# Performance work log

Hardware: AMD Instinct MI355X
Metric: run time of the kernel (lower is better)

## Reference

```python
import jax, jax.numpy as jnp
import numpy as np

B, NB, C, FEAT = 2, 512, 80, 1024
FIRST_N = 128
NMS_FC = 128
POS_EMB = 64
GROUPS = 16
ATT_D = (1024, 1024, 128)
NUM_THRESH = 3
BBOX_W = (10.0, 10.0, 5.0, 5.0)
SCALE_CLAMP = float(np.log(1000.0 / 16.0))


def setup_inputs() -> dict:
    key = jax.random.key(0)
    ks = jax.random.split(key, 24)
    roi_feat = jax.random.normal(ks[0], (B * NB, FEAT), jnp.float32)
    scores = jax.random.normal(ks[1], (B * NB, C + 1), jnp.float32)
    proposal_deltas = jax.random.normal(ks[2], (B * NB, C * 4), jnp.float32) * 0.5
    xy = jax.random.uniform(ks[3], (B * NB, 2), jnp.float32) * 800.0
    wh = jax.random.uniform(ks[4], (B * NB, 2), jnp.float32) * 100.0 + 1.0
    proposal_boxes = jnp.concatenate([xy, xy + wh], axis=1)

    def lin(k, fin, fout, std=0.01):
        return jax.random.normal(k, (fin, fout), jnp.float32) * std

    return {
        'roi_feat': roi_feat,
        'scores': scores,
        'proposal_deltas': proposal_deltas,
        'proposal_boxes': proposal_boxes,
        'roi_w': lin(ks[5], FEAT, NMS_FC), 'roi_b': jnp.zeros((NMS_FC,), jnp.float32),
        'rank_w': lin(ks[6], FEAT, NMS_FC), 'rank_b': jnp.zeros((NMS_FC,), jnp.float32),
        'logit_w': lin(ks[7], NMS_FC, NUM_THRESH), 'logit_b': jnp.full((NUM_THRESH,), -3.0, jnp.float32),
        'pos_w': lin(ks[8], POS_EMB, GROUPS), 'pos_b': jnp.zeros((GROUPS,), jnp.float32),
        'q_w': lin(ks[9], NMS_FC, ATT_D[0]), 'q_b': jnp.zeros((ATT_D[0],), jnp.float32),
        'k_w': lin(ks[10], NMS_FC, ATT_D[1]), 'k_b': jnp.zeros((ATT_D[1],), jnp.float32),
        'out_w': jax.random.normal(ks[11], (GROUPS, NMS_FC, ATT_D[2] // GROUPS), jnp.float32) * 0.01,
        'out_b': jnp.zeros((ATT_D[2],), jnp.float32),
        'num_boxes': NB,
    }


def _rank_embedding():
    # sinusoidal rank embedding, dim FEAT
    fr = jnp.arange(FEAT // 2, dtype=jnp.float32)
    dim_mat = jnp.power(1000.0, (2.0 / FEAT) * fr)
    div = jnp.arange(FIRST_N, dtype=jnp.float32)[:, None] / dim_mat[None, :]
    return jnp.concatenate([jnp.sin(div), jnp.cos(div)], axis=1)  # (FIRST_N, FEAT)


def _pos_embed(boxes):
    # boxes: (FIRST_N, C, 4) -> (C, N, N, POS_EMB)
    b = jnp.transpose(boxes, (1, 0, 2))  # (C, N, 4)
    x1, y1, x2, y2 = b[..., 0], b[..., 1], b[..., 2], b[..., 3]
    w = x2 - x1 + 1.0
    h = y2 - y1 + 1.0
    cx = 0.5 * (x1 + x2)
    cy = 0.5 * (y1 + y2)
    dx = jnp.log(jnp.maximum(jnp.abs((cx[:, :, None] - cx[:, None, :]) / w[:, :, None]), 1e-3))
    dy = jnp.log(jnp.maximum(jnp.abs((cy[:, :, None] - cy[:, None, :]) / h[:, :, None]), 1e-3))
    dw = jnp.log(w[:, :, None] / w[:, None, :])
    dh = jnp.log(h[:, :, None] / h[:, None, :])
    pm = jnp.stack([dx, dy, dw, dh], axis=-1)  # (C, N, N, 4)
    fr = jnp.arange(POS_EMB // 8, dtype=jnp.float32)
    dim_mat = jnp.power(1000.0, (8.0 / POS_EMB) * fr)
    dv = (pm * 100.0)[..., None] / dim_mat  # (C, N, N, 4, POS_EMB//8)
    e = jnp.concatenate([jnp.sin(dv), jnp.cos(dv)], axis=-1)  # (C, N, N, 4, POS_EMB//4)
    return e.reshape(pm.shape[:3] + (POS_EMB,))


def reference(roi_feat, scores, proposal_deltas, proposal_boxes,
              roi_w, roi_b, rank_w, rank_b, logit_w, logit_b,
              pos_w, pos_b, q_w, q_b, k_w, k_b, out_w, out_b, num_boxes):
    deltas = jax.lax.stop_gradient(proposal_deltas)  # detached in original
    pboxes = jax.lax.stop_gradient(proposal_boxes)
    batch = deltas.shape[0] // num_boxes

    # ---- Box2BoxTransform.apply_deltas ----
    widths = pboxes[:, 2] - pboxes[:, 0]
    heights = pboxes[:, 3] - pboxes[:, 1]
    ctr_x = pboxes[:, 0] + 0.5 * widths
    ctr_y = pboxes[:, 1] + 0.5 * heights
    wx, wy, ww, wh = BBOX_W
    d = deltas.reshape(-1, C, 4)
    dx = d[..., 0] / wx
    dy = d[..., 1] / wy
    dw = jnp.minimum(d[..., 2] / ww, SCALE_CLAMP)
    dh = jnp.minimum(d[..., 3] / wh, SCALE_CLAMP)
    pcx = dx * widths[:, None] + ctr_x[:, None]
    pcy = dy * heights[:, None] + ctr_y[:, None]
    pw = jnp.exp(dw) * widths[:, None]
    ph = jnp.exp(dh) * heights[:, None]
    refined = jnp.stack([pcx - 0.5 * pw, pcy - 0.5 * ph, pcx + 0.5 * pw, pcy + 0.5 * ph], axis=-1)
    refined = refined.reshape(batch, num_boxes, C, 4)

    # ---- softmax + per-class descending sort, keep first_n ----
    sc = scores.reshape(batch, num_boxes, C + 1)
    probs = jax.nn.softmax(sc[..., :C], axis=1)
    rank_idxs = jnp.argsort(-probs, axis=1)[:, :FIRST_N, :]  # (B, FIRST_N, C)
    sorted_score = jnp.take_along_axis(probs, rank_idxs, axis=1)  # (B, FIRST_N, C)
    sorted_boxes = jax.vmap(lambda bx, i: jnp.take_along_axis(bx, i[..., None], axis=0))(refined, rank_idxs)  # (B, FIRST_N, C, 4)

    # ---- rank + roi embeddings ----
    rank_feat = _rank_embedding() @ rank_w + rank_b  # (FIRST_N, NMS_FC)
    roi_emb = (roi_feat @ roi_w + roi_b).reshape(batch, num_boxes, NMS_FC)
    sorted_roi = jax.vmap(lambda e, i: e[i])(roi_emb, rank_idxs)  # (B, FIRST_N, C, NMS_FC)
    emb_feat = sorted_roi + rank_feat[None, :, None, :]

    dq = ATT_D[0] // GROUPS
    dk = ATT_D[1] // GROUPS

    def attend(feat, boxes):
        # feat: (FIRST_N, C, NMS_FC), boxes: (FIRST_N, C, 4)
        pe = _pos_embed(boxes)  # (C, N, N, POS_EMB)
        aff_w = jax.nn.relu(pe @ pos_w + pos_b)  # (C, N, N, G)
        aff_w = jnp.transpose(aff_w, (0, 3, 1, 2))  # (C, G, N, N)
        f = jnp.transpose(feat, (1, 0, 2))  # (C, N, NMS_FC)
        q = (f @ q_w + q_b).reshape(C, FIRST_N, GROUPS, dq).transpose(0, 2, 1, 3)
        k = (f @ k_w + k_b).reshape(C, FIRST_N, GROUPS, dk).transpose(0, 2, 1, 3)
        aff = jnp.einsum('cgnd,cgmd->cgnm', q, k) / jnp.sqrt(jnp.float32(dk))
        sm = jax.nn.softmax(jnp.log(jnp.maximum(aff_w, 1e-6)) + aff, axis=-1)
        ov = jnp.einsum('cgnm,cmd->cgnd', sm, f)  # (C, G, N, NMS_FC)
        lin = jnp.einsum('cgnd,gde->cnge', ov, out_w).reshape(C, FIRST_N, ATT_D[2]) + out_b
        return jnp.transpose(lin, (1, 0, 2))  # (N, C, ATT_D[2])

    att = jax.vmap(attend)(emb_feat, sorted_boxes)
    all_feat = jax.nn.relu(emb_feat + att)
    logit = all_feat @ logit_w + logit_b  # (B, FIRST_N, C, NUM_THRESH)
    nms_multi_score = jax.nn.sigmoid(logit) * sorted_score[..., None]
    return nms_multi_score
```

## Files before the change

kernel.cpp:

```cpp
#include <hip/hip_runtime.h>
#include <math.h>

#define B_    2
#define NB_   512
#define C_    80
#define FEAT_ 1024
#define FN_   128
#define FC_   128
#define PE_   64
#define G_    16
#define DQ_   64
#define EO_   8
#define NT_   3
#define SCALE_CLAMP_ 4.135166556742356f

typedef __attribute__((ext_vector_type(8))) short bf16x8;
typedef __attribute__((ext_vector_type(4))) float f32x4;

#define O_ROIP    ((size_t)0)
#define O_RANKP   (O_ROIP + (size_t)2*B_*NB_*FC_)
#define O_RANKIDX (O_RANKP + (size_t)2*FN_*FC_)
#define O_SSCORE  (O_RANKIDX + (size_t)B_*FN_*C_)
#define O_SBOX    (O_SSCORE + (size_t)B_*FN_*C_)
#define O_EMB     (O_SBOX + (size_t)B_*FN_*C_*4)
#define O_ATT     (O_EMB + (size_t)B_*FN_*C_*FC_)
#define O_LW      (O_ATT + (size_t)B_*FN_*C_*FC_)

__device__ __forceinline__ float bf2f(unsigned short u) {
    return __uint_as_float(((unsigned int)u) << 16);
}
__device__ __forceinline__ unsigned short f2bf(float f) {
    unsigned int x = __float_as_uint(f);
    unsigned int r = (x + 0x7fff + ((x >> 16) & 1)) >> 16;
    return (unsigned short)r;
}

#define ADDR128(row, gr)  ((row)*128 + ((((gr) ^ ((row)&7))) << 4))
#define ADDR256(row, gr)  ((row)*256 + ((((gr) ^ ((row)&15))) << 4))

__global__ __launch_bounds__(256) void k_embed(const float* __restrict__ roi_feat,
                                               const float* __restrict__ roi_w,
                                               const float* __restrict__ roi_b,
                                               const float* __restrict__ rank_w,
                                               const float* __restrict__ rank_b,
                                               float* __restrict__ roiP,
                                               float* __restrict__ rankP)
{
    const int bid = blockIdx.x;
    const int kh  = bid & 1;
    const int rt  = bid >> 1;
    const bool isRank = rt >= 64;
    const int row0 = (isRank ? rt - 64 : rt) * 16;
    const int t = threadIdx.x;
    const int w = t >> 6, lane = t & 63, lr = lane & 15, lh = lane >> 4;
    const int col0 = w * 32;
    const float* W = isRank ? rank_w : roi_w;
    const float* bias = isRank ? rank_b : roi_b;

    const int arow = row0 + lr;
    f32x4 acc0 = {0,0,0,0}, acc1 = {0,0,0,0};

    #pragma unroll 4
    for (int ks = 0; ks < 16; ++ks) {
        const int kb = kh*512 + ks*32 + lh*8;
        bf16x8 af;
        if (!isRank) {
            float4 a0 = *(const float4*)(roi_feat + (size_t)arow*FEAT_ + kb);
            float4 a1 = *(const float4*)(roi_feat + (size_t)arow*FEAT_ + kb + 4);
            af[0] = (short)f2bf(a0.x); af[1] = (short)f2bf(a0.y);
            af[2] = (short)f2bf(a0.z); af[3] = (short)f2bf(a0.w);
            af[4] = (short)f2bf(a1.x); af[5] = (short)f2bf(a1.y);
            af[6] = (short)f2bf(a1.z); af[7] = (short)f2bf(a1.w);
        } else {
            #pragma unroll
            for (int j = 0; j < 8; ++j) {
                int k = kb + j;
                int kk = k & 511;
                float inv = exp2f(-(float)kk * 0.0194644226f);
                float arg = (float)arow * inv;
                float v = (k < 512) ? __sinf(arg) : __cosf(arg);
                af[j] = (short)f2bf(v);
            }
        }
        bf16x8 bf0, bf1;
        #pragma unroll
        for (int j = 0; j < 8; ++j) {
            const float* wr = W + (size_t)(kb + j)*FC_ + col0 + lr;
            bf0[j] = (short)f2bf(wr[0]);
            bf1[j] = (short)f2bf(wr[16]);
        }
        acc0 = __builtin_amdgcn_mfma_f32_16x16x32_bf16(af, bf0, acc0, 0, 0, 0);
        acc1 = __builtin_amdgcn_mfma_f32_16x16x32_bf16(af, bf1, acc1, 0, 0, 0);
    }
    float* dst = isRank ? (rankP + (size_t)kh*FN_*FC_) : (roiP + (size_t)kh*(B_*NB_)*FC_);
    #pragma unroll
    for (int tile = 0; tile < 2; ++tile) {
        f32x4 a = tile ? acc1 : acc0;
        int col = col0 + tile*16 + lr;
        float bv = (kh == 0) ? bias[col] : 0.0f;
        #pragma unroll
        for (int reg = 0; reg < 4; ++reg) {
            int rr = row0 + lh*4 + reg;
            dst[(size_t)rr*FC_ + col] = a[reg] + bv;
        }
    }
}

__global__ __launch_bounds__(512) void k_topk(const float* __restrict__ scores,
                                              int* __restrict__ rank_idx,
                                              float* __restrict__ sorted_score)
{
    int b = blockIdx.x / C_, c = blockIdx.x % C_;
    __shared__ float p[NB_];
    __shared__ float red[NB_];
    int i = threadIdx.x;
    float s = scores[(size_t)(b*NB_ + i)*(C_+1) + c];
    red[i] = s; __syncthreads();
    for (int o = 256; o > 0; o >>= 1) { if (i < o) red[i] = fmaxf(red[i], red[i+o]); __syncthreads(); }
    float mx = red[0]; __syncthreads();
    float e = expf(s - mx);
    red[i] = e; __syncthreads();
    for (int o = 256; o > 0; o >>= 1) { if (i < o) red[i] += red[i+o]; __syncthreads(); }
    float sum = red[0]; __syncthreads();
    float pi = e / sum;
    p[i] = pi; __syncthreads();
    int rank = 0;
    for (int j = 0; j < NB_; ++j) {
        float pj = p[j];
        rank += (pj > pi) || (pj == pi && j < i);
    }
    if (rank < FN_) {
        rank_idx[(size_t)(b*FN_ + rank)*C_ + c] = i;
        sorted_score[(size_t)(b*FN_ + rank)*C_ + c] = pi;
    }
}

__global__ __launch_bounds__(256) void k_gather(const int* __restrict__ rank_idx,
                                                const float* __restrict__ roiP,
                                                const float* __restrict__ rankP,
                                                const float* __restrict__ pdeltas,
                                                const float* __restrict__ pboxes,
                                                float* __restrict__ emb_feat,
                                                float* __restrict__ sorted_boxes)
{
    const int t = threadIdx.x;
    const int item = blockIdx.x*8 + (t >> 5);
    const int l = t & 31;
    const int c = item % C_;
    const int bn = item / C_;
    const int n = bn & (FN_-1);
    const int b = bn >> 7;
    const int idx = rank_idx[item];
    const int row = b*NB_ + idx;
    float4 e0 = *(const float4*)(roiP + (size_t)row*FC_ + l*4);
    float4 e1 = *(const float4*)(roiP + (size_t)(B_*NB_ + row)*FC_ + l*4);
    float4 r0 = *(const float4*)(rankP + (size_t)n*FC_ + l*4);
    float4 r1 = *(const float4*)(rankP + (size_t)(FN_ + n)*FC_ + l*4);
    *(float4*)(emb_feat + (size_t)item*FC_ + l*4) =
        make_float4(e0.x+e1.x+r0.x+r1.x, e0.y+e1.y+r0.y+r1.y,
                    e0.z+e1.z+r0.z+r1.z, e0.w+e1.w+r0.w+r1.w);
    if (l == 0) {
        float x1 = pboxes[row*4+0], y1 = pboxes[row*4+1], x2 = pboxes[row*4+2], y2 = pboxes[row*4+3];
        float w = x2 - x1, h = y2 - y1;
        float cx = x1 + 0.5f*w, cy = y1 + 0.5f*h;
        const float* dl = pdeltas + (size_t)row*(C_*4) + c*4;
        float dx = dl[0]/10.0f, dy = dl[1]/10.0f;
        float dw = fminf(dl[2]/5.0f, SCALE_CLAMP_);
        float dh = fminf(dl[3]/5.0f, SCALE_CLAMP_);
        float pcx = dx*w + cx, pcy = dy*h + cy;
        float pw = expf(dw)*w, ph = expf(dh)*h;
        float* ob = sorted_boxes + (size_t)item*4;
        ob[0] = pcx - 0.5f*pw; ob[1] = pcy - 0.5f*ph;
        ob[2] = pcx + 0.5f*pw; ob[3] = pcy + 0.5f*ph;
    }
}

__global__ __launch_bounds__(256) void k_pos2(const float* __restrict__ sorted_boxes,
                                              const float* __restrict__ pos_w,
                                              const float* __restrict__ pos_b,
                                              unsigned short* __restrict__ lw)
{
    const int n2   = blockIdx.x & 63;
    const int rest = blockIdx.x >> 6;
    const int cl   = rest % C_;
    const int b    = rest / C_;
    const int n0   = n2 * 2;
    const int t    = threadIdx.x;

    __shared__ float geomL[FN_][6];
    __shared__ unsigned short featL[256*PE_];
    __shared__ unsigned short poswL[G_*PE_];
    __shared__ float pbL[G_];
    __shared__ float sdimL[8];

    if (t < FN_) {
        const float* bx = sorted_boxes + (((size_t)(b*FN_ + t))*C_ + cl)*4;
        float x1 = bx[0], y1 = bx[1], x2 = bx[2], y2 = bx[3];
        float w = x2 - x1 + 1.0f;
        float h = y2 - y1 + 1.0f;
        geomL[t][0] = 0.5f*(x1+x2);
        geomL[t][1] = 0.5f*(y1+y2);
        geomL[t][2] = w;
        geomL[t][3] = h;
        geomL[t][4] = __logf(w);
        geomL[t][5] = __logf(h);
    } else {
        int id = t - 128;
        int g  = id >> 3;
        int gr = id & 7;
        unsigned short u[8];
        #pragma unroll
        for (int j = 0; j < 8; ++j) u[j] = f2bf(pos_w[(gr*8 + j)*G_ + g]);
        *(uint4*)((char*)poswL + ADDR128(g, gr)) =
            make_uint4((unsigned)u[0] | ((unsigned)u[1] << 16),
                       (unsigned)u[2] | ((unsigned)u[3] << 16),
                       (unsigned)u[4] | ((unsigned)u[5] << 16),
                       (unsigned)u[6] | ((unsigned)u[7] << 16));
    }
    if (t < G_) pbL[t] = pos_b[t];
    if (t >= 16 && t < 24) sdimL[t-16] = 1.0f / powf(1000.0f, 0.125f*(float)(t-16));
    __syncthreads();

    {
        const int nl = t >> 7;
        const int m  = t & 127;
        const int n  = n0 + nl;
        float pm[4];
        {
            float cxn = geomL[n][0], cyn = geomL[n][1];
            float rwn = 1.0f/geomL[n][2], rhn = 1.0f/geomL[n][3];
            pm[0] = __logf(fmaxf(fabsf((cxn - geomL[m][0]) * rwn), 1e-3f)) * 100.0f;
            pm[1] = __logf(fmaxf(fabsf((cyn - geomL[m][1]) * rhn), 1e-3f)) * 100.0f;
            pm[2] = (geomL[n][4] - geomL[m][4]) * 100.0f;
            pm[3] = (geomL[n][5] - geomL[m][5]) * 100.0f;
        }
        char* base = (char*)featL;
        #pragma unroll
        for (int f = 0; f < 4; ++f) {
            float s[8], c[8];
            #pragma unroll
            for (int r = 0; r < 8; ++r) {
                __sincosf(pm[f] * sdimL[r], &s[r], &c[r]);
            }
            unsigned short us[8], uc[8];
            #pragma unroll
            for (int r = 0; r < 8; ++r) { us[r] = f2bf(s[r]); uc[r] = f2bf(c[r]); }
            *(uint4*)(base + ADDR128(t, 2*f)) =
                make_uint4((unsigned)us[0] | ((unsigned)us[1] << 16),
                           (unsigned)us[2] | ((unsigned)us[3] << 16),
                           (unsigned)us[4] | ((unsigned)us[5] << 16),
                           (unsigned)us[6] | ((unsigned)us[7] << 16));
            *(uint4*)(base + ADDR128(t, 2*f + 1)) =
                make_uint4((unsigned)uc[0] | ((unsigned)uc[1] << 16),
                           (unsigned)uc[2] | ((unsigned)uc[3] << 16),
                           (unsigned)uc[4] | ((unsigned)uc[5] << 16),
                           (unsigned)uc[6] | ((unsigned)uc[7] << 16));
        }
    }
    __syncthreads();

    {
        const int wave = t >> 6, lane = t & 63;
        const int lr = lane & 15, lh = lane >> 4;
        const float pbg = pbL[lr];
        #pragma unroll
        for (int ti = 0; ti < 4; ++ti) {
            const int t16 = wave*4 + ti;
            f32x4 acc = {0,0,0,0};
            #pragma unroll
            for (int ks = 0; ks < 2; ++ks) {
                bf16x8 a  = *(const bf16x8*)((char*)featL + ADDR128(t16*16 + lr, ks*4 + lh));
                bf16x8 bb = *(const bf16x8*)((char*)poswL + ADDR128(lr, ks*4 + lh));
                acc = __builtin_amdgcn_mfma_f32_16x16x32_bf16(a, bb, acc, 0, 0, 0);
            }
            const int g = lr;
            #pragma unroll
            for (int reg = 0; reg < 4; ++reg) {
                int p = t16*16 + lh*4 + reg;
                int n = n0 + (p >> 7);
                int m = p & 127;
                float w = fmaxf(fmaxf(acc[reg] + pbg, 0.0f), 1e-6f);
                lw[(((size_t)(b*C_ + cl)*FN_ + n)*G_ + g)*FN_ + m] = f2bf(w);
            }
        }
    }
}

#define FT_OFF   0
#define QL_OFF   32768
#define KL_OFF   49152
#define WT_OFF   65536
#define AFF_OFF  65536
#define VT_OFF   133632
#define BIAS_OFF 137728
#define SMEM_SZ  138240

__global__ __launch_bounds__(1024) void k_attn(const float* __restrict__ emb_feat,
                                               const float* __restrict__ q_w, const float* __restrict__ q_b,
                                               const float* __restrict__ k_w, const float* __restrict__ k_b,
                                               const float* __restrict__ out_w, const float* __restrict__ out_b,
                                               const unsigned short* __restrict__ lw,
                                               float* __restrict__ att)
{
    const int g    = blockIdx.x & 15;
    const int rest = blockIdx.x >> 4;
    const int cl   = rest % C_;
    const int b    = rest / C_;
    const int c    = cl;
    const int t  = threadIdx.x;
    const int wave = t >> 6;
    const int lane = t & 63;
    const int lr = lane & 15;
    const int lh = lane >> 4;

    __shared__ char smem[SMEM_SZ];
    float* biasL = (float*)(smem + BIAS_OFF);
    float* affF  = (float*)(smem + AFF_OFF);

    for (int s = 0; s < 4; ++s) {
        int fi = t + s*1024;
        int n  = fi >> 5;
        int d4 = (fi & 31) << 2;
        float4 v = *(const float4*)(emb_feat + ((size_t)(b*FN_ + n)*C_ + c)*FC_ + d4);
        char* dst = smem + FT_OFF + ADDR256(n, d4 >> 3) + ((d4 >> 2) & 1)*8;
        *(uint2*)dst = make_uint2((unsigned)f2bf(v.x) | ((unsigned)f2bf(v.y) << 16),
                                  (unsigned)f2bf(v.z) | ((unsigned)f2bf(v.w) << 16));
    }
    for (int s = 0; s < 2; ++s) {
        int id = t + s*1024;
        int r  = id & 127;
        int g8 = id >> 7;
        const float* src = (r < 64) ? (q_w + (size_t)(g8*8)*1024 + g*DQ_ + r)
                                    : (k_w + (size_t)(g8*8)*1024 + g*DQ_ + (r-64));
        unsigned short u[8];
        #pragma unroll
        for (int j = 0; j < 8; ++j) u[j] = f2bf(src[(size_t)j*1024]);
        char* dst = smem + WT_OFF + ADDR256(r, g8);
        *(uint4*)dst = make_uint4((unsigned)u[0] | ((unsigned)u[1] << 16),
                                  (unsigned)u[2] | ((unsigned)u[3] << 16),
                                  (unsigned)u[4] | ((unsigned)u[5] << 16),
                                  (unsigned)u[6] | ((unsigned)u[7] << 16));
    }
    if (t < 128) {
        int e  = t & 7;
        int g8 = t >> 3;
        const float* src = out_w + (size_t)g*FC_*EO_ + (size_t)(g8*8)*EO_ + e;
        unsigned short u[8];
        #pragma unroll
        for (int j = 0; j < 8; ++j) u[j] = f2bf(src[(size_t)j*EO_]);
        int r = 128 + e;
        char* dst = smem + WT_OFF + ADDR256(r, g8);
        *(uint4*)dst = make_uint4((unsigned)u[0] | ((unsigned)u[1] << 16),
                                  (unsigned)u[2] | ((unsigned)u[3] << 16),
                                  (unsigned)u[4] | ((unsigned)u[5] << 16),
                                  (unsigned)u[6] | ((unsigned)u[7] << 16));
    }
    if (t >= 256 && t < 512) {
        int i = t - 256;
        *(uint2*)(smem + WT_OFF + 136*256 + i*8) = make_uint2(0u, 0u);
    }
    if (t >= 512 && t < 768) {
        int i = t - 512;
        *(uint2*)(smem + VT_OFF + 8*256 + i*8) = make_uint2(0u, 0u);
    }
    if (t >= 128 && t < 256) {
        int r = t - 128;
        biasL[r] = (r < 64) ? q_b[g*DQ_ + r] : k_b[g*DQ_ + (r-64)];
    }
    __syncthreads();

    {
        const int rb = (wave >> 2) * 32;
        const int nb = (wave & 3) * 32;
        f32x4 acc00 = {0,0,0,0}, acc01 = {0,0,0,0}, acc10 = {0,0,0,0}, acc11 = {0,0,0,0};
        f32x4 accV  = {0,0,0,0};
        #pragma unroll
        for (int ks = 0; ks < 4; ++ks) {
            int soff = ((ks*4 + lh) ^ lr) << 4;
            bf16x8 a0 = *(const bf16x8*)(smem + WT_OFF + (rb + lr)*256 + soff);
            bf16x8 a1 = *(const bf16x8*)(smem + WT_OFF + (rb + 16 + lr)*256 + soff);
            bf16x8 b0 = *(const bf16x8*)(smem + FT_OFF + (nb + lr)*256 + soff);
            bf16x8 b1 = *(const bf16x8*)(smem + FT_OFF + (nb + 16 + lr)*256 + soff);
            acc00 = __builtin_amdgcn_mfma_f32_16x16x32_bf16(a0, b0, acc00, 0, 0, 0);
            acc01 = __builtin_amdgcn_mfma_f32_16x16x32_bf16(a0, b1, acc01, 0, 0, 0);
            acc10 = __builtin_amdgcn_mfma_f32_16x16x32_bf16(a1, b0, acc10, 0, 0, 0);
            acc11 = __builtin_amdgcn_mfma_f32_16x16x32_bf16(a1, b1, acc11, 0, 0, 0);
            if (wave < 8) {
                bf16x8 av = *(const bf16x8*)(smem + WT_OFF + (128 + lr)*256 + soff);
                bf16x8 bv = *(const bf16x8*)(smem + FT_OFF + (wave*16 + lr)*256 + soff);
                accV = __builtin_amdgcn_mfma_f32_16x16x32_bf16(av, bv, accV, 0, 0, 0);
            }
        }
        #pragma unroll
        for (int ti = 0; ti < 2; ++ti) {
            #pragma unroll
            for (int tj = 0; tj < 2; ++tj) {
                f32x4 a = (ti == 0) ? (tj == 0 ? acc00 : acc01) : (tj == 0 ? acc10 : acc11);
                int r0 = rb + ti*16 + lh*4;
                int n  = nb + tj*16 + lr;
                float v0 = a[0] + biasL[r0+0];
                float v1 = a[1] + biasL[r0+1];
                float v2 = a[2] + biasL[r0+2];
                float v3 = a[3] + biasL[r0+3];
                int dq0 = r0 & 63;
                int off = (r0 < 64 ? QL_OFF : KL_OFF);
                char* dst = smem + off + ADDR128(n, dq0 >> 3) + ((dq0 >> 2) & 1)*8;
                *(uint2*)dst = make_uint2((unsigned)f2bf(v0) | ((unsigned)f2bf(v1) << 16),
                                          (unsigned)f2bf(v2) | ((unsigned)f2bf(v3) << 16));
            }
        }
        if (wave < 8 && lh < 2) {
            int m = wave*16 + lr;
            #pragma unroll
            for (int reg = 0; reg < 4; ++reg) {
                int e = lh*4 + reg;
                char* dst = smem + VT_OFF + (e)*256 + ((((m >> 3) ^ e)) << 4) + (m & 7)*2;
                *(unsigned short*)dst = f2bf(accV[reg]);
            }
        }
    }
    __syncthreads();

    {
        const int nb = (wave >> 2) * 32;
        const int mb = (wave & 3) * 32;
        f32x4 acc00 = {0,0,0,0}, acc01 = {0,0,0,0}, acc10 = {0,0,0,0}, acc11 = {0,0,0,0};
        #pragma unroll
        for (int ks = 0; ks < 2; ++ks) {
            int soff = ((ks*4 + lh) ^ (lr & 7)) << 4;
            bf16x8 a0 = *(const bf16x8*)(smem + QL_OFF + (nb + lr)*128 + soff);
            bf16x8 a1 = *(const bf16x8*)(smem + QL_OFF + (nb + 16 + lr)*128 + soff);
            bf16x8 b0 = *(const bf16x8*)(smem + KL_OFF + (mb + lr)*128 + soff);
            bf16x8 b1 = *(const bf16x8*)(smem + KL_OFF + (mb + 16 + lr)*128 + soff);
            acc00 = __builtin_amdgcn_mfma_f32_16x16x32_bf16(a0, b0, acc00, 0, 0, 0);
            acc01 = __builtin_amdgcn_mfma_f32_16x16x32_bf16(a0, b1, acc01, 0, 0, 0);
            acc10 = __builtin_amdgcn_mfma_f32_16x16x32_bf16(a1, b0, acc10, 0, 0, 0);
            acc11 = __builtin_amdgcn_mfma_f32_16x16x32_bf16(a1, b1, acc11, 0, 0, 0);
        }
        #pragma unroll
        for (int ti = 0; ti < 2; ++ti) {
            #pragma unroll
            for (int tj = 0; tj < 2; ++tj) {
                f32x4 a = (ti == 0) ? (tj == 0 ? acc00 : acc01) : (tj == 0 ? acc10 : acc11);
                int n0 = nb + ti*16 + lh*4;
                int m  = mb + tj*16 + lr;
                #pragma unroll
                for (int reg = 0; reg < 4; ++reg)
                    affF[(n0 + reg)*133 + m] = a[reg];
            }
        }
    }
    __syncthreads();

    {
        const int row = t >> 3;
        const int lp  = t & 7;
        const int m0  = lp * 16;
        const unsigned short* lwrow = lw + ((((size_t)(b*C_ + cl))*FN_ + row)*G_ + g)*FN_ + m0;
        float v[16];
        float mx = -INFINITY;
        #pragma unroll
        for (int j = 0; j < 16; ++j) {
            float val = affF[row*133 + m0 + j]*0.125f + __logf(bf2f(lwrow[j]));
            v[j] = val;
            mx = fmaxf(mx, val);
        }
        #pragma unroll
        for (int s = 1; s < 8; s <<= 1) mx = fmaxf(mx, __shfl_xor(mx, s, 8));
        float sum = 0.f;
        #pragma unroll
        for (int j = 0; j < 16; ++j) { v[j] = __expf(v[j] - mx); sum += v[j]; }
        #pragma unroll
        for (int s = 1; s < 8; s <<= 1) sum += __shfl_xor(sum, s, 8);
        float rs = 1.0f / sum;
        unsigned short u[16];
        #pragma unroll
        for (int j = 0; j < 16; ++j) u[j] = f2bf(v[j] * rs);
        char* d0 = smem + FT_OFF + ADDR256(row, lp*2);
        char* d1 = smem + FT_OFF + ADDR256(row, lp*2 + 1);
        *(uint4*)d0 = make_uint4((unsigned)u[0] | ((unsigned)u[1] << 16),
                                 (unsigned)u[2] | ((unsigned)u[3] << 16),
                                 (unsigned)u[4] | ((unsigned)u[5] << 16),
                                 (unsigned)u[6] | ((unsigned)u[7] << 16));
        *(uint4*)d1 = make_uint4((unsigned)u[8]  | ((unsigned)u[9]  << 16),
                                 (unsigned)u[10] | ((unsigned)u[11] << 16),
                                 (unsigned)u[12] | ((unsigned)u[13] << 16),
                                 (unsigned)u[14] | ((unsigned)u[15] << 16));
    }
    __syncthreads();

    if (wave < 8) {
        const int tb = wave * 16;
        f32x4 acc = {0,0,0,0};
        #pragma unroll
        for (int ks = 0; ks < 4; ++ks) {
            int soff = ((ks*4 + lh) ^ lr) << 4;
            bf16x8 a = *(const bf16x8*)(smem + FT_OFF + (tb + lr)*256 + soff);
            bf16x8 bv = *(const bf16x8*)(smem + VT_OFF + lr*256 + soff);
            acc = __builtin_amdgcn_mfma_f32_16x16x32_bf16(a, bv, acc, 0, 0, 0);
        }
        if (lr < 8) {
            float ob = out_b[g*EO_ + lr];
            #pragma unroll
            for (int reg = 0; reg < 4; ++reg) {
                int n = tb + lh*4 + reg;
                att[((size_t)(b*FN_ + n)*C_ + c)*FC_ + g*EO_ + lr] = acc[reg] + ob;
            }
        }
    }
}

__global__ __launch_bounds__(256) void k_final(const float* __restrict__ emb_feat,
                                               const float* __restrict__ att,
                                               const float* __restrict__ logit_w,
                                               const float* __restrict__ logit_b,
                                               const float* __restrict__ sorted_score,
                                               float* __restrict__ out)
{
    __shared__ float lwL[FC_*NT_ + NT_];
    const int t = threadIdx.x;
    for (int i = t; i < FC_*NT_ + NT_; i += 256)
        lwL[i] = (i < FC_*NT_) ? logit_w[i] : logit_b[i - FC_*NT_];
    __syncthreads();
    const int item = blockIdx.x*8 + (t >> 5);
    const int l = t & 31;
    const int d0 = l*4;
    float4 ev = *(const float4*)(emb_feat + (size_t)item*FC_ + d0);
    float4 av = *(const float4*)(att + (size_t)item*FC_ + d0);
    float a0 = fmaxf(ev.x + av.x, 0.f);
    float a1 = fmaxf(ev.y + av.y, 0.f);
    float a2 = fmaxf(ev.z + av.z, 0.f);
    float a3 = fmaxf(ev.w + av.w, 0.f);
    float s0 = a0*lwL[(d0+0)*NT_+0] + a1*lwL[(d0+1)*NT_+0] + a2*lwL[(d0+2)*NT_+0] + a3*lwL[(d0+3)*NT_+0];
    float s1 = a0*lwL[(d0+0)*NT_+1] + a1*lwL[(d0+1)*NT_+1] + a2*lwL[(d0+2)*NT_+1] + a3*lwL[(d0+3)*NT_+1];
    float s2 = a0*lwL[(d0+0)*NT_+2] + a1*lwL[(d0+1)*NT_+2] + a2*lwL[(d0+2)*NT_+2] + a3*lwL[(d0+3)*NT_+2];
    #pragma unroll
    for (int s = 1; s < 32; s <<= 1) {
        s0 += __shfl_xor(s0, s, 32);
        s1 += __shfl_xor(s1, s, 32);
        s2 += __shfl_xor(s2, s, 32);
    }
    if (l < NT_) {
        float lg = (l == 0) ? s0 : (l == 1) ? s1 : s2;
        lg += lwL[FC_*NT_ + l];
        float sg = 1.f / (1.f + expf(-lg));
        out[(size_t)item*NT_ + l] = sg * sorted_score[item];
    }
}

extern "C" void kernel_launch(void* const* d_in, const int* in_sizes, int n_in,
                              void* d_out, int out_size, void* d_ws, size_t ws_size,
                              hipStream_t stream) {
    (void)in_sizes; (void)n_in; (void)out_size; (void)ws_size;
    const float* roi_feat = (const float*)d_in[0];
    const float* scores   = (const float*)d_in[1];
    const float* pdeltas  = (const float*)d_in[2];
    const float* pboxes   = (const float*)d_in[3];
    const float* roi_w    = (const float*)d_in[4];
    const float* roi_b    = (const float*)d_in[5];
    const float* rank_w   = (const float*)d_in[6];
    const float* rank_b   = (const float*)d_in[7];
    const float* logit_w  = (const float*)d_in[8];
    const float* logit_b  = (const float*)d_in[9];
    const float* pos_w    = (const float*)d_in[10];
    const float* pos_b    = (const float*)d_in[11];
    const float* q_w      = (const float*)d_in[12];
    const float* q_b      = (const float*)d_in[13];
    const float* k_w      = (const float*)d_in[14];
    const float* k_b      = (const float*)d_in[15];
    const float* out_w    = (const float*)d_in[16];
    const float* out_b    = (const float*)d_in[17];
    float* ws = (float*)d_ws;

    float* roiP         = ws + O_ROIP;
    float* rankP        = ws + O_RANKP;
    int*   rank_idx     = (int*)(ws + O_RANKIDX);
    float* sorted_score = ws + O_SSCORE;
    float* sorted_boxes = ws + O_SBOX;
    float* emb_feat     = ws + O_EMB;
    float* att          = ws + O_ATT;
    unsigned short* lwb = (unsigned short*)(ws + O_LW);

    k_embed<<<dim3(144), dim3(256), 0, stream>>>(roi_feat, roi_w, roi_b, rank_w, rank_b,
                                                 roiP, rankP);
    k_topk<<<dim3(B_*C_), dim3(512), 0, stream>>>(scores, rank_idx, sorted_score);
    k_gather<<<dim3(B_*FN_*C_/8), dim3(256), 0, stream>>>(rank_idx, roiP, rankP,
                                                          pdeltas, pboxes, emb_feat, sorted_boxes);
    k_pos2<<<dim3(B_*C_*64), dim3(256), 0, stream>>>(sorted_boxes, pos_w, pos_b, lwb);
    k_attn<<<dim3(B_*C_*G_), dim3(1024), 0, stream>>>(emb_feat, q_w, q_b, k_w, k_b,
                                                      out_w, out_b, lwb, att);
    k_final<<<dim3(B_*FN_*C_/8), dim3(256), 0, stream>>>(emb_feat, att, logit_w, logit_b,
                                                         sorted_score, d_out ? (float*)d_out : nullptr);
}
```

Baseline: 180.3 us.

## Shrink attention LDS footprint and precompute log position weights in fp16

The attention kernel no longer stages Q/K/out weights in shared memory. Each wave now loads those weights straight from global memory into MFMA operands. The feature tile moves to a padded 272-byte row layout, and the fp32 affinity scratch becomes fp16 stored in the same buffer, cutting LDS from about 138KB to about 72KB so more blocks can be resident. The position-weight kernel now stores log(w) as fp16 instead of bf16 w, which takes the log out of the softmax inner loop and vectorises the loads. The rank loop also reads the shared scores as float4. The costs are repeated uncoalesced global weight loads per wave and fp16 range and precision risk on the affinities.

```diff
diff --git a/kernel.cpp b/kernel.cpp
--- a/kernel.cpp
+++ b/kernel.cpp
@@ -34,9 +34,16 @@
     unsigned int r = (x + 0x7fff + ((x >> 16) & 1)) >> 16;
     return (unsigned short)r;
 }
+__device__ __forceinline__ unsigned short f2h(float x) {
+    _Float16 h = (_Float16)x;
+    return __builtin_bit_cast(unsigned short, h);
+}
+__device__ __forceinline__ float h2f(unsigned short u) {
+    _Float16 h = __builtin_bit_cast(_Float16, u);
+    return (float)h;
+}
 
 #define ADDR128(row, gr)  ((row)*128 + ((((gr) ^ ((row)&7))) << 4))
-#define ADDR256(row, gr)  ((row)*256 + ((((gr) ^ ((row)&15))) << 4))
 
 __global__ __launch_bounds__(256) void k_embed(const float* __restrict__ roi_feat,
                                                const float* __restrict__ roi_w,
@@ -125,9 +132,13 @@
     float pi = e / sum;
     p[i] = pi; __syncthreads();
     int rank = 0;
-    for (int j = 0; j < NB_; ++j) {
-        float pj = p[j];
-        rank += (pj > pi) || (pj == pi && j < i);
+    for (int j4 = 0; j4 < NB_/4; ++j4) {
+        float4 pj = *(const float4*)&p[j4*4];
+        int j = j4*4;
+        rank += (pj.x > pi) || (pj.x == pi && (j+0) < i);
+        rank += (pj.y > pi) || (pj.y == pi && (j+1) < i);
+        rank += (pj.z > pi) || (pj.z == pi && (j+2) < i);
+        rank += (pj.w > pi) || (pj.w == pi && (j+3) < i);
     }
     if (rank < FN_) {
         rank_idx[(size_t)(b*FN_ + rank)*C_ + c] = i;
@@ -280,22 +291,20 @@
                 int n = n0 + (p >> 7);
                 int m = p & 127;
                 float w = fmaxf(fmaxf(acc[reg] + pbg, 0.0f), 1e-6f);
-                lw[(((size_t)(b*C_ + cl)*FN_ + n)*G_ + g)*FN_ + m] = f2bf(w);
+                lw[(((size_t)(b*C_ + cl)*FN_ + n)*G_ + g)*FN_ + m] = f2h(__logf(w));
             }
         }
     }
 }
 
 #define FT_OFF   0
-#define QL_OFF   32768
-#define KL_OFF   49152
-#define WT_OFF   65536
-#define AFF_OFF  65536
-#define VT_OFF   133632
-#define BIAS_OFF 137728
-#define SMEM_SZ  138240
-
-__global__ __launch_bounds__(1024) void k_attn(const float* __restrict__ emb_feat,
+#define QL_OFF   34816
+#define KL_OFF   51200
+#define VT_OFF   67584
+#define BIAS_OFF 71680
+#define SMEM_SZ  72192
+
+__global__ __launch_bounds__(1024, 8) void k_attn(const float* __restrict__ emb_feat,
                                                const float* __restrict__ q_w, const float* __restrict__ q_b,
                                                const float* __restrict__ k_w, const float* __restrict__ k_b,
                                                const float* __restrict__ out_w, const float* __restrict__ out_b,
@@ -315,49 +324,15 @@
 
     __shared__ char smem[SMEM_SZ];
     float* biasL = (float*)(smem + BIAS_OFF);
-    float* affF  = (float*)(smem + AFF_OFF);
 
     for (int s = 0; s < 4; ++s) {
         int fi = t + s*1024;
         int n  = fi >> 5;
         int d4 = (fi & 31) << 2;
         float4 v = *(const float4*)(emb_feat + ((size_t)(b*FN_ + n)*C_ + c)*FC_ + d4);
-        char* dst = smem + FT_OFF + ADDR256(n, d4 >> 3) + ((d4 >> 2) & 1)*8;
+        char* dst = smem + FT_OFF + n*272 + (fi & 31)*8;
         *(uint2*)dst = make_uint2((unsigned)f2bf(v.x) | ((unsigned)f2bf(v.y) << 16),
                                   (unsigned)f2bf(v.z) | ((unsigned)f2bf(v.w) << 16));
-    }
-    for (int s = 0; s < 2; ++s) {
-        int id = t + s*1024;
-        int r  = id & 127;
-        int g8 = id >> 7;
-        const float* src = (r < 64) ? (q_w + (size_t)(g8*8)*1024 + g*DQ_ + r)
-                                    : (k_w + (size_t)(g8*8)*1024 + g*DQ_ + (r-64));
-        unsigned short u[8];
-        #pragma unroll
-        for (int j = 0; j < 8; ++j) u[j] = f2bf(src[(size_t)j*1024]);
-        char* dst = smem + WT_OFF + ADDR256(r, g8);
-        *(uint4*)dst = make_uint4((unsigned)u[0] | ((unsigned)u[1] << 16),
-                                  (unsigned)u[2] | ((unsigned)u[3] << 16),
-                                  (unsigned)u[4] | ((unsigned)u[5] << 16),
-                                  (unsigned)u[6] | ((unsigned)u[7] << 16));
-    }
-    if (t < 128) {
-        int e  = t & 7;
-        int g8 = t >> 3;
-        const float* src = out_w + (size_t)g*FC_*EO_ + (size_t)(g8*8)*EO_ + e;
-        unsigned short u[8];
-        #pragma unroll
-        for (int j = 0; j < 8; ++j) u[j] = f2bf(src[(size_t)j*EO_]);
-        int r = 128 + e;
-        char* dst = smem + WT_OFF + ADDR256(r, g8);
-        *(uint4*)dst = make_uint4((unsigned)u[0] | ((unsigned)u[1] << 16),
-                                  (unsigned)u[2] | ((unsigned)u[3] << 16),
-                                  (unsigned)u[4] | ((unsigned)u[5] << 16),
-                                  (unsigned)u[6] | ((unsigned)u[7] << 16));
-    }
-    if (t >= 256 && t < 512) {
-        int i = t - 256;
-        *(uint2*)(smem + WT_OFF + 136*256 + i*8) = make_uint2(0u, 0u);
     }
     if (t >= 512 && t < 768) {
         int i = t - 512;
@@ -372,22 +347,33 @@
     {
         const int rb = (wave >> 2) * 32;
         const int nb = (wave & 3) * 32;
+        const float* wsrc = (rb < 64) ? q_w : k_w;
+        const int col0 = g*DQ_ + (rb & 63) + lr;
         f32x4 acc00 = {0,0,0,0}, acc01 = {0,0,0,0}, acc10 = {0,0,0,0}, acc11 = {0,0,0,0};
         f32x4 accV  = {0,0,0,0};
         #pragma unroll
         for (int ks = 0; ks < 4; ++ks) {
-            int soff = ((ks*4 + lh) ^ lr) << 4;
-            bf16x8 a0 = *(const bf16x8*)(smem + WT_OFF + (rb + lr)*256 + soff);
-            bf16x8 a1 = *(const bf16x8*)(smem + WT_OFF + (rb + 16 + lr)*256 + soff);
-            bf16x8 b0 = *(const bf16x8*)(smem + FT_OFF + (nb + lr)*256 + soff);
-            bf16x8 b1 = *(const bf16x8*)(smem + FT_OFF + (nb + 16 + lr)*256 + soff);
+            const int k0 = ks*32 + lh*8;
+            bf16x8 a0, a1;
+            #pragma unroll
+            for (int j = 0; j < 8; ++j) {
+                const float* kp = wsrc + (size_t)(k0 + j)*1024;
+                a0[j] = (short)f2bf(kp[col0]);
+                a1[j] = (short)f2bf(kp[col0 + 16]);
+            }
+            const int fo = ks*64 + lh*16;
+            bf16x8 b0 = *(const bf16x8*)(smem + FT_OFF + (nb + lr)*272 + fo);
+            bf16x8 b1 = *(const bf16x8*)(smem + FT_OFF + (nb + 16 + lr)*272 + fo);
             acc00 = __builtin_amdgcn_mfma_f32_16x16x32_bf16(a0, b0, acc00, 0, 0, 0);
             acc01 = __builtin_amdgcn_mfma_f32_16x16x32_bf16(a0, b1, acc01, 0, 0, 0);
             acc10 = __builtin_amdgcn_mfma_f32_16x16x32_bf16(a1, b0, acc10, 0, 0, 0);
             acc11 = __builtin_amdgcn_mfma_f32_16x16x32_bf16(a1, b1, acc11, 0, 0, 0);
             if (wave < 8) {
-                bf16x8 av = *(const bf16x8*)(smem + WT_OFF + (128 + lr)*256 + soff);
-                bf16x8 bv = *(const bf16x8*)(smem + FT_OFF + (wave*16 + lr)*256 + soff);
+                bf16x8 av;
+                #pragma unroll
+                for (int j = 0; j < 8; ++j)
+                    av[j] = (lr < 8) ? (short)f2bf(out_w[(size_t)g*1024 + (size_t)(k0 + j)*8 + lr]) : (short)0;
+                bf16x8 bv = *(const bf16x8*)(smem + FT_OFF + (wave*16 + lr)*272 + fo);
                 accV = __builtin_amdgcn_mfma_f32_16x16x32_bf16(av, bv, accV, 0, 0, 0);
             }
         }
@@ -446,7 +432,7 @@
                 int m  = mb + tj*16 + lr;
                 #pragma unroll
                 for (int reg = 0; reg < 4; ++reg)
-                    affF[(n0 + reg)*133 + m] = a[reg];
+                    *(unsigned short*)(smem + FT_OFF + (n0 + reg)*272 + 2*m) = f2h(a[reg]);
             }
         }
     }
@@ -457,13 +443,26 @@
         const int lp  = t & 7;
         const int m0  = lp * 16;
         const unsigned short* lwrow = lw + ((((size_t)(b*C_ + cl))*FN_ + row)*G_ + g)*FN_ + m0;
+        uint4 gl0 = *(const uint4*)(lwrow);
+        uint4 gl1 = *(const uint4*)(lwrow + 8);
+        char* abase = smem + FT_OFF + row*272 + lp*32;
+        uint4 af0 = *(const uint4*)abase;
+        uint4 af1 = *(const uint4*)(abase + 16);
+        const unsigned short* ah0 = (const unsigned short*)&af0;
+        const unsigned short* ah1 = (const unsigned short*)&af1;
+        const unsigned short* lp0 = (const unsigned short*)&gl0;
+        const unsigned short* lp1 = (const unsigned short*)&gl1;
         float v[16];
         float mx = -INFINITY;
         #pragma unroll
-        for (int j = 0; j < 16; ++j) {
-            float val = affF[row*133 + m0 + j]*0.125f + __logf(bf2f(lwrow[j]));
-            v[j] = val;
-            mx = fmaxf(mx, val);
+        for (int j = 0; j < 8; ++j) {
+            float val = h2f(ah0[j])*0.125f + h2f(lp0[j]);
+            v[j] = val; mx = fmaxf(mx, val);
+        }
+        #pragma unroll
+        for (int j = 0; j < 8; ++j) {
+            float val = h2f(ah1[j])*0.125f + h2f(lp1[j]);
+            v[8+j] = val; mx = fmaxf(mx, val);
         }
         #pragma unroll
         for (int s = 1; s < 8; s <<= 1) mx = fmaxf(mx, __shfl_xor(mx, s, 8));
@@ -476,16 +475,14 @@
         unsigned short u[16];
         #pragma unroll
         for (int j = 0; j < 16; ++j) u[j] = f2bf(v[j] * rs);
-        char* d0 = smem + FT_OFF + ADDR256(row, lp*2);
-        char* d1 = smem + FT_OFF + ADDR256(row, lp*2 + 1);
-        *(uint4*)d0 = make_uint4((unsigned)u[0] | ((unsigned)u[1] << 16),
-                                 (unsigned)u[2] | ((unsigned)u[3] << 16),
-                                 (unsigned)u[4] | ((unsigned)u[5] << 16),
-                                 (unsigned)u[6] | ((unsigned)u[7] << 16));
-        *(uint4*)d1 = make_uint4((unsigned)u[8]  | ((unsigned)u[9]  << 16),
-                                 (unsigned)u[10] | ((unsigned)u[11] << 16),
-                                 (unsigned)u[12] | ((unsigned)u[13] << 16),
-                                 (unsigned)u[14] | ((unsigned)u[15] << 16));
+        *(uint4*)abase = make_uint4((unsigned)u[0] | ((unsigned)u[1] << 16),
+                                    (unsigned)u[2] | ((unsigned)u[3] << 16),
+                                    (unsigned)u[4] | ((unsigned)u[5] << 16),
+                                    (unsigned)u[6] | ((unsigned)u[7] << 16));
+        *(uint4*)(abase + 16) = make_uint4((unsigned)u[8]  | ((unsigned)u[9]  << 16),
+                                           (unsigned)u[10] | ((unsigned)u[11] << 16),
+                                           (unsigned)u[12] | ((unsigned)u[13] << 16),
+                                           (unsigned)u[14] | ((unsigned)u[15] << 16));
     }
     __syncthreads();
 
@@ -494,8 +491,9 @@
         f32x4 acc = {0,0,0,0};
         #pragma unroll
         for (int ks = 0; ks < 4; ++ks) {
+            const int fo = ks*64 + lh*16;
             int soff = ((ks*4 + lh) ^ lr) << 4;
-            bf16x8 a = *(const bf16x8*)(smem + FT_OFF + (tb + lr)*256 + soff);
+            bf16x8 a = *(const bf16x8*)(smem + FT_OFF + (tb + lr)*272 + fo);
             bf16x8 bv = *(const bf16x8*)(smem + VT_OFF + lr*256 + soff);
             acc = __builtin_amdgcn_mfma_f32_16x16x32_bf16(a, bv, acc, 0, 0, 0);
         }
```

After: 188.3 us. 1.04x slower.
